# Kernel optimization log

Measured on AMD Instinct MI355X. Metric: run time of the kernel, lower is better.

The kernel has to match this reference:

```python
import jax, jax.numpy as jnp
import numpy as np
from jax import lax

K = 3  # deform kernel size (forced by shape consistency of the offset branch)


def conv2d(x, w, b, pad):
    y = lax.conv_general_dilated(x, w, (1, 1), [(pad, pad), (pad, pad)],
                                 dimension_numbers=('NCHW', 'OIHW', 'NCHW'))
    return y + b[None, :, None, None]


def deform_conv(x, offset, w):
    # Deformable conv v1, stride 1, pad 0, per-group offsets, zero outside borders.
    B, Cin, H, W = x.shape
    Cout = w.shape[0]
    Ho, Wo = H - K + 1, W - K + 1
    G = offset.shape[1] // (2 * K * K)  # num deformable groups (= cin // c_p_g)
    cpg = Cin // G
    # offset layout: [B, G, K*K, 2(y,x), Ho, Wo]
    off = offset.reshape(B, G, K * K, 2, Ho, Wo)
    ky = (jnp.arange(K * K) // K).astype(x.dtype)
    kx = (jnp.arange(K * K) % K).astype(x.dtype)
    py = off[:, :, :, 0] + jnp.arange(Ho, dtype=x.dtype)[None, None, None, :, None] + ky[None, None, :, None, None]
    px = off[:, :, :, 1] + jnp.arange(Wo, dtype=x.dtype)[None, None, None, None, :] + kx[None, None, :, None, None]
    y0 = jnp.floor(py)
    x0 = jnp.floor(px)
    fy = (py - y0)[..., None]  # [B,G,KK,Ho,Wo,1]
    fx = (px - x0)[..., None]
    y0i = y0.astype(jnp.int32)
    x0i = x0.astype(jnp.int32)
    xr = x.reshape(B, G, cpg, H, W)
    bi = jnp.arange(B)[:, None, None, None, None]
    gi = jnp.arange(G)[None, :, None, None, None]

    def gather(iy, ix):
        valid = (iy >= 0) & (iy < H) & (ix >= 0) & (ix < W)
        v = xr[bi, gi, :, jnp.clip(iy, 0, H - 1), jnp.clip(ix, 0, W - 1)]  # [B,G,KK,Ho,Wo,cpg]
        return v * valid[..., None].astype(x.dtype)

    v = ((1 - fy) * (1 - fx) * gather(y0i, x0i)
         + (1 - fy) * fx * gather(y0i, x0i + 1)
         + fy * (1 - fx) * gather(y0i + 1, x0i)
         + fy * fx * gather(y0i + 1, x0i + 1))
    # [B,G,KK,Ho,Wo,cpg] -> [B, Cin*K*K, Ho, Wo] matching weight layout [Cout, Cin, K, K]
    cols = v.transpose(0, 1, 5, 2, 3, 4).reshape(B, Cin * K * K, Ho, Wo)
    return jnp.einsum('ok,bkhw->bohw', w.reshape(Cout, -1), cols)


def setup_inputs() -> dict:
    key = jax.random.key(0)
    ks = jax.random.split(key, 8)
    B, cin, cout, H, W = 4, 64, 64, 130, 130
    s = 0.05
    x = jax.random.normal(ks[0], (B, cin, H, W), jnp.float32)
    w0 = jax.random.normal(ks[1], (cin, cin, 3, 3), jnp.float32) * s
    b0 = jnp.zeros((cin,), jnp.float32)
    w1 = jax.random.normal(ks[2], (cin // 2, cin, 1, 1), jnp.float32) * s
    b1 = jnp.zeros((cin // 2,), jnp.float32)
    w2 = jax.random.normal(ks[3], (cin // 2, cin // 2, 3, 3), jnp.float32) * s
    b2 = jnp.zeros((cin // 2,), jnp.float32)
    off_ch = cin * 2 * K * K  # c_p_g = 1 -> G = cin
    w3 = jax.random.normal(ks[4], (off_ch, cin // 2, 1, 1), jnp.float32) * s
    b3 = jnp.zeros((off_ch,), jnp.float32)
    wd = jax.random.normal(ks[5], (cout, cin, K, K), jnp.float32) * s
    return {"x": x, "w0": w0, "b0": b0, "w1": w1, "b1": b1, "w2": w2, "b2": b2,
            "w3": w3, "b3": b3, "wd": wd}


def reference(x, w0, b0, w1, b1, w2, b2, w3, b3, wd):
    t = conv2d(x, w0, b0, 0)                                   # [B,cin,H-2,W-2]
    t = lax.reduce_window(t, -jnp.inf, lax.max, (1, 1, 2, 2), (1, 1, 2, 2), 'VALID')
    t = conv2d(t, w1, b1, 0)
    t = conv2d(t, w2, b2, 1)
    t = conv2d(t, w3, b3, 0)                                   # offset logits
    t = jnp.repeat(jnp.repeat(t, 2, axis=2), 2, axis=3)        # nearest x2 upsample
    return deform_conv(x, t, wd)
```

## Files before the change

kernel.cpp:

```cpp
#include <hip/hip_runtime.h>
#include <hip/hip_bf16.h>
#include <hip/hip_fp16.h>


#define HX 130
#define WX 130

typedef short bf16x8 __attribute__((ext_vector_type(8)));
typedef _Float16 f16x8 __attribute__((ext_vector_type(8)));
typedef float f32x4 __attribute__((ext_vector_type(4)));

static __device__ __forceinline__ unsigned short f2bf(float f) {
    unsigned u = __float_as_uint(f);
    unsigned r = u + 0x7fff + ((u >> 16) & 1);
    return (unsigned short)(r >> 16);
}

static __device__ __forceinline__ int aoff320(int row, int col) {
    return row * 320 + ((((col >> 3) ^ (row & 7))) << 3) + (col & 7);
}

static __device__ __forceinline__ int aoff192(int row, int col) {
    return row * 192 + ((((col >> 3) ^ (row & 7))) << 3) + (col & 7);
}

__global__ __launch_bounds__(256) void k_wdt(const float* __restrict__ wd,
                                             const float* __restrict__ w3,
                                             const float* __restrict__ w0,
                                             const float* __restrict__ w2,
                                             unsigned short* __restrict__ wdtb,
                                             __half* __restrict__ w3h,
                                             unsigned short* __restrict__ w0b,
                                             unsigned short* __restrict__ w2b) {
    int idx = blockIdx.x * 256 + threadIdx.x;
    if (idx < 36864) {
        int o = idx / 576;
        int rem = idx - o * 576;
        int c = rem / 9;
        int kk = rem - c * 9;
        int h = c >> 5;
        int c5 = c & 31;
        int col = (c5 >> 4) * 144 + ((c5 >> 3) & 1) * 72 + (c5 & 7) * 9 + kk;
        wdtb[(size_t)(h * 64 + o) * 288 + col] = f2bf(wd[idx]);
        if (idx < 16) wdtb[36864 + idx] = 0;
    } else if (idx < 73728) {
        int i2 = idx - 36864;
        w3h[i2] = __float2half_rn(w3[i2]);
    } else if (idx < 114688) {
        int i3 = idx - 73728;
        int row = i3 / 160;
        int col = i3 - row * 160;
        int cig = row >> 6, oc = row & 63;
        unsigned short v = 0;
        if (col < 144) {
            int ci = (col * 57) >> 9;
            int kk = col - ci * 9;
            v = f2bf(w0[(size_t)(oc * 64 + cig * 16 + ci) * 9 + kk]);
        }
        w0b[i3] = v;
    } else {
        int i4 = idx - 114688;
        int row = i4 / 160;
        int col = i4 - row * 160;
        int cig = row >> 5, oc = row & 31;
        unsigned short v = 0;
        if (col < 144) {
            int ci = (col * 57) >> 9;
            int kk = col - ci * 9;
            v = f2bf(w2[(size_t)(oc * 32 + cig * 16 + ci) * 9 + kk]);
        }
        w2b[i4] = v;
    }
}

__global__ __launch_bounds__(256, 4) void k_conv0_mfma(const float* __restrict__ x,
                                                       const unsigned short* __restrict__ w0b,
                                                       const float* __restrict__ b0,
                                                       float* __restrict__ p1) {
    int blk = blockIdx.x;
    int tx = blk & 15;
    int ty = (blk >> 4) & 15;
    int b = blk >> 8;
    int tid = threadIdx.x;
    int w = tid >> 6;
    int lane = tid & 63;
    int lm = lane & 15;
    int lq = lane >> 4;
    int oy0 = ty * 8, ox0 = tx * 8;

    __shared__ __align__(16) unsigned short alds[64 * 192];
    __shared__ __align__(16) float xlds[1600];

    f32x4 acc[4];
    #pragma unroll
    for (int n = 0; n < 4; ++n) acc[n] = (f32x4){0.f, 0.f, 0.f, 0.f};

    if (tid < 128) {
        *(bf16x8*)&alds[aoff192(tid >> 1, 144 + (tid & 1) * 8)] =
            (bf16x8){0, 0, 0, 0, 0, 0, 0, 0};
    }

    const float* xb = x + (size_t)(b * 64) * (HX * WX) + oy0 * WX + ox0;
    int apx = tid >> 2;
    int acq = tid & 3;
    int py = apx >> 3, pxx = apx & 7;

    for (int cig = 0; cig < 4; ++cig) {
        #pragma unroll
        for (int j = 0; j < 7; ++j) {
            int i = tid + j * 256;
            if (i < 1600) {
                int ci = i / 100;
                int rem = i - ci * 100;
                int rr = rem / 10, cc = rem - rr * 10;
                xlds[i] = xb[(size_t)(cig * 16 + ci) * (HX * WX) + rr * WX + cc];
            }
        }
        __syncthreads();
        #pragma unroll
        for (int jj = 0; jj < 36; ++jj) {
            int col = acq * 36 + jj;
            int ci = (col * 57) >> 9;
            int kk = col - ci * 9;
            int ky = kk / 3, kx = kk - ky * 3;
            alds[aoff192(apx, col)] =
                f2bf(xlds[ci * 100 + (py + ky) * 10 + (pxx + kx)]);
        }
        __syncthreads();
        int arow = w * 16 + lm;
        const unsigned short* bbase = w0b + (size_t)cig * 64 * 160;
        #pragma unroll
        for (int ks = 0; ks < 5; ++ks) {
            bf16x8 a = *(const bf16x8*)&alds[aoff192(arow, ks * 32 + lq * 8)];
            #pragma unroll
            for (int n = 0; n < 4; ++n) {
                bf16x8 bb = *(const bf16x8*)(bbase + (size_t)(n * 16 + lm) * 160
                                             + ks * 32 + lq * 8);
                acc[n] = __builtin_amdgcn_mfma_f32_16x16x32_bf16(a, bb, acc[n], 0, 0, 0);
            }
        }
    }

    __syncthreads();
    float* dlds = (float*)alds;
    #pragma unroll
    for (int n = 0; n < 4; ++n) {
        int oc = n * 16 + lm;
        #pragma unroll
        for (int r = 0; r < 4; ++r) {
            int px = w * 16 + lq * 4 + r;
            dlds[oc * 65 + px] = acc[n][r];
        }
    }
    __syncthreads();
    {
        int oc = tid >> 2;
        int ppy = tid & 3;
        float bo = b0[oc];
        float4 o4;
        #pragma unroll
        for (int ppx = 0; ppx < 4; ++ppx) {
            const float* dp = &dlds[oc * 65 + (2 * ppy) * 8 + 2 * ppx];
            float m = fmaxf(fmaxf(dp[0], dp[1]), fmaxf(dp[8], dp[9])) + bo;
            ((float*)&o4)[ppx] = m;
        }
        *(float4*)(p1 + (((size_t)b * 64 + oc) * 64 + ty * 4 + ppy) * 64 + tx * 4) = o4;
    }
}

__global__ __launch_bounds__(256) void k_conv1x1_a(const float* __restrict__ p1,
                                                   const float* __restrict__ w1,
                                                   const float* __restrict__ b1,
                                                   float* __restrict__ t2) {
    int blk = blockIdx.x;
    int qt = blk & 3;
    int cog = (blk >> 2) & 15;
    int b = blk >> 6;
    int q = qt * 256 + threadIdx.x;
    float4 acc[2];
    #pragma unroll
    for (int i = 0; i < 2; ++i) {
        float bv = b1[cog * 2 + i];
        acc[i] = make_float4(bv, bv, bv, bv);
    }
    const float* ip = p1 + (size_t)b * 64 * 4096 + q * 4;
    for (int ci = 0; ci < 64; ++ci) {
        float4 v = *(const float4*)(ip + (size_t)ci * 4096);
        #pragma unroll
        for (int i = 0; i < 2; ++i) {
            float wv = w1[(cog * 2 + i) * 64 + ci];
            acc[i].x += wv * v.x; acc[i].y += wv * v.y;
            acc[i].z += wv * v.z; acc[i].w += wv * v.w;
        }
    }
    float* op = t2 + (size_t)b * 32 * 4096 + q * 4;
    #pragma unroll
    for (int i = 0; i < 2; ++i)
        *(float4*)(op + (size_t)(cog * 2 + i) * 4096) = acc[i];
}

__global__ __launch_bounds__(256, 4) void k_conv3_mfma(const float* __restrict__ t2,
                                                       const unsigned short* __restrict__ w2b,
                                                       const float* __restrict__ b2,
                                                       float* __restrict__ t3) {
    int blk = blockIdx.x;
    int tx = blk & 7;
    int ty = (blk >> 3) & 7;
    int b = blk >> 6;
    int tid = threadIdx.x;
    int w = tid >> 6;
    int lane = tid & 63;
    int lm = lane & 15;
    int lq = lane >> 4;
    int oy0 = ty * 8, ox0 = tx * 8;

    __shared__ __align__(16) unsigned short alds[64 * 192];
    __shared__ __align__(16) float xlds[1600];

    f32x4 acc[2];
    #pragma unroll
    for (int n = 0; n < 2; ++n) acc[n] = (f32x4){0.f, 0.f, 0.f, 0.f};

    if (tid < 128) {
        *(bf16x8*)&alds[aoff192(tid >> 1, 144 + (tid & 1) * 8)] =
            (bf16x8){0, 0, 0, 0, 0, 0, 0, 0};
    }

    const float* tb = t2 + (size_t)(b * 32) * 4096;
    int apx = tid >> 2;
    int acq = tid & 3;
    int py = apx >> 3, pxx = apx & 7;

    for (int cig = 0; cig < 2; ++cig) {
        #pragma unroll
        for (int j = 0; j < 7; ++j) {
            int i = tid + j * 256;
            if (i < 1600) {
                int ci = i / 100;
                int rem = i - ci * 100;
                int rr = rem / 10, cc = rem - rr * 10;
                int gy = oy0 + rr - 1, gx = ox0 + cc - 1;
                bool ok = (gy >= 0) & (gy < 64) & (gx >= 0) & (gx < 64);
                xlds[i] = ok ? tb[(size_t)(cig * 16 + ci) * 4096 + gy * 64 + gx]
                             : 0.f;
            }
        }
        __syncthreads();
        #pragma unroll
        for (int jj = 0; jj < 36; ++jj) {
            int col = acq * 36 + jj;
            int ci = (col * 57) >> 9;
            int kk = col - ci * 9;
            int ky = kk / 3, kx = kk - ky * 3;
            alds[aoff192(apx, col)] =
                f2bf(xlds[ci * 100 + (py + ky) * 10 + (pxx + kx)]);
        }
        __syncthreads();
        int arow = w * 16 + lm;
        const unsigned short* bbase = w2b + (size_t)cig * 32 * 160;
        #pragma unroll
        for (int ks = 0; ks < 5; ++ks) {
            bf16x8 a = *(const bf16x8*)&alds[aoff192(arow, ks * 32 + lq * 8)];
            #pragma unroll
            for (int n = 0; n < 2; ++n) {
                bf16x8 bb = *(const bf16x8*)(bbase + (size_t)(n * 16 + lm) * 160
                                             + ks * 32 + lq * 8);
                acc[n] = __builtin_amdgcn_mfma_f32_16x16x32_bf16(a, bb, acc[n], 0, 0, 0);
            }
        }
    }

    __syncthreads();
    float* dlds = (float*)alds;
    #pragma unroll
    for (int n = 0; n < 2; ++n) {
        int oc = n * 16 + lm;
        #pragma unroll
        for (int r = 0; r < 4; ++r) {
            int px = w * 16 + lq * 4 + r;
            dlds[oc * 65 + px] = acc[n][r];
        }
    }
    __syncthreads();
    {
        int oc = tid >> 3;
        int r = tid & 7;
        float bo = b2[oc];
        const float* dp = &dlds[oc * 65 + r * 8];
        float* op = t3 + ((size_t)(b * 32 + oc) * 64 + oy0 + r) * 64 + ox0;
        float4 a4 = make_float4(dp[0] + bo, dp[1] + bo, dp[2] + bo, dp[3] + bo);
        float4 b4 = make_float4(dp[4] + bo, dp[5] + bo, dp[6] + bo, dp[7] + bo);
        *(float4*)(op) = a4;
        *(float4*)(op + 4) = b4;
    }
}

__global__ __launch_bounds__(256, 3) void k_deform(const float* __restrict__ x,
                                                   const float* __restrict__ t3,
                                                   const __half* __restrict__ w3h,
                                                   const float* __restrict__ b3,
                                                   const unsigned short* __restrict__ wdtb,
                                                   float* __restrict__ out) {
    int blk = blockIdx.x;
    int b = blk & 3;
    int strip = blk >> 2;
    int tid = threadIdx.x;
    int po0 = strip * 16;
    int qy = po0 >> 6;
    int qx0 = po0 & 63;
    int w = tid >> 6;
    int lane = tid & 63;
    int lm = lane & 15;
    int lq = lane >> 4;
    int tq = tid & 15;
    int kb = tid >> 4;

    __shared__ __align__(16) unsigned short alds[64 * 320];
    __shared__ __align__(16) __half2 soff[2304];
    __shared__ __align__(16) _Float16 st3t[16 * 40];

    f32x4 acc[4];
    #pragma unroll
    for (int n = 0; n < 4; ++n) acc[n] = (f32x4){0.f, 0.f, 0.f, 0.f};

    const float* xb = x + (size_t)b * 64 * HX * WX;
    float fybase = (float)(2 * qy);
    float fxbase = (float)(2 * (qx0 + tq));

    {
        int px = tid & 15, ci0 = tid >> 4;
        const float* t3p = t3 + (size_t)b * 32 * 4096 + (qy * 64 + qx0 + px);
        st3t[px * 40 + ci0]      = (_Float16)t3p[(size_t)ci0 * 4096];
        st3t[px * 40 + ci0 + 16] = (_Float16)t3p[(size_t)(ci0 + 16) * 4096];
    }
    __syncthreads();
    const f16x8 bfrag = *(const f16x8*)&st3t[lm * 40 + lq * 8];

    for (int h = 0; h < 2; ++h) {
        #pragma unroll 1
        for (int sl = 0; sl < 2; ++sl) {
            int s = h * 2 + sl;
            __syncthreads();

            #pragma unroll
            for (int rep = 0; rep < 5; ++rep) {
                int t = rep * 4 + w;
                if (rep == 4) { if (w >= 2) break; t = 16 + w; }
                const f16x8 afrag = *(const f16x8*)((const _Float16*)w3h
                        + (size_t)(s * 288 + t * 16 + lm) * 32 + lq * 8);
                f32x4 d = __builtin_amdgcn_mfma_f32_16x16x32_f16(
                        afrag, bfrag, (f32x4){0.f, 0.f, 0.f, 0.f}, 0, 0, 0);
                float4 bq = *(const float4*)(b3 + s * 288 + t * 16 + lq * 4);
                int p0 = (t * 8 + lq * 2) * 16 + lm;
                soff[p0]      = __floats2half2_rn(d[0] + bq.x, d[1] + bq.y);
                soff[p0 + 16] = __floats2half2_rn(d[2] + bq.z, d[3] + bq.w);
            }
            __syncthreads();

            __half2 o2h[9];
            #pragma unroll
            for (int it = 0; it < 9; ++it)
                o2h[it] = soff[it * 256 + tid];
            #pragma unroll
            for (int it = 0; it < 9; ++it) {
                int kcol = it * 16 + kb;
                int lc = kcol >= 72;
                int ckk = kcol - 72 * lc;
                int ch = (ckk * 57) >> 9;
                int kk = ckk - ch * 9;
                int c = s * 16 + lc * 8 + ch;
                int clocal = sl * 144 + kcol;
                float2 off = __half22float2(o2h[it]);
                float py = off.x + fybase + (float)(kk / 3);
                float px = off.y + fxbase + (float)(kk % 3);
                float y0f = floorf(py), x0f = floorf(px);
                float fy = py - y0f, fx = px - x0f;
                int y0 = (int)y0f, x0 = (int)x0f;
                const float* xp = xb + (size_t)c * (HX * WX);
                float tv[3][3];
                bool fastok = (y0 >= 0) & (y0 <= HX - 3) & (x0 >= 0) & (x0 <= WX - 3);
                if (__all(fastok)) {
                    int xe = x0 & ~1;
                    int odd = x0 & 1;
                    const float* rp = xp + y0 * WX + xe;
                    #pragma unroll
                    for (int r = 0; r < 3; ++r) {
                        float2 A = *(const float2*)(rp);
                        float2 B = *(const float2*)(rp + 2);
                        tv[r][0] = odd ? A.y : A.x;
                        tv[r][1] = odd ? B.x : A.y;
                        tv[r][2] = odd ? B.y : B.x;
                        rp += WX;
                    }
                } else {
                    #pragma unroll
                    for (int r = 0; r < 3; ++r) {
                        int yy = y0 + r;
                        bool vy = (yy >= 0) & (yy < HX);
                        int yc = min(max(yy, 0), HX - 1);
                        #pragma unroll
                        for (int sx = 0; sx < 3; ++sx) {
                            int xx = x0 + sx;
                            bool vx = (xx >= 0) & (xx < WX);
                            int xc = min(max(xx, 0), WX - 1);
                            float val = xp[yc * WX + xc];
                            tv[r][sx] = (vy & vx) ? val : 0.f;
                        }
                    }
                }
                float h0[3], h1[3];
                #pragma unroll
                for (int r = 0; r < 3; ++r) {
                    h0[r] = tv[r][0] + fx * (tv[r][1] - tv[r][0]);
                    h1[r] = tv[r][1] + fx * (tv[r][2] - tv[r][1]);
                }
                alds[aoff320(0 * 16 + tq, clocal)] = f2bf(h0[0] + fy * (h0[1] - h0[0]));
                alds[aoff320(1 * 16 + tq, clocal)] = f2bf(h1[0] + fy * (h1[1] - h1[0]));
                alds[aoff320(2 * 16 + tq, clocal)] = f2bf(h0[1] + fy * (h0[2] - h0[1]));
                alds[aoff320(3 * 16 + tq, clocal)] = f2bf(h1[1] + fy * (h1[2] - h1[1]));
            }
        }
        __syncthreads();

        int arow = w * 16 + lm;
        const unsigned short* bbase = wdtb + (size_t)(h * 64) * 288;
        #pragma unroll
        for (int ks = 0; ks < 9; ++ks) {
            bf16x8 a = *(const bf16x8*)&alds[aoff320(arow, ks * 32 + lq * 8)];
            #pragma unroll
            for (int n = 0; n < 4; ++n) {
                bf16x8 bb = *(const bf16x8*)(bbase + (size_t)(n * 16 + lm) * 288
                                             + ks * 32 + lq * 8);
                acc[n] = __builtin_amdgcn_mfma_f32_16x16x32_bf16(a, bb, acc[n], 0, 0, 0);
            }
        }
    }

    __syncthreads();
    float* dlds = (float*)alds;
    #pragma unroll
    for (int n = 0; n < 4; ++n) {
        int oc = n * 16 + lm;
        #pragma unroll
        for (int r = 0; r < 4; ++r) {
            int px = w * 16 + lq * 4 + r;
            dlds[oc * 65 + px] = acc[n][r];
        }
    }
    __syncthreads();
    {
        int oc = tid >> 2;
        int sy = (tid >> 1) & 1;
        int qh = (tid & 1) * 8;
        float* orow = out + (((size_t)b * 64 + oc) * 128 + 2 * qy + sy) * 128 + 2 * qx0;
        const float* d0 = &dlds[oc * 65 + (sy * 2 + 0) * 16];
        const float* d1 = &dlds[oc * 65 + (sy * 2 + 1) * 16];
        #pragma unroll
        for (int i = 0; i < 8; ++i) {
            int q = qh + i;
            *(float2*)(orow + 2 * q) = make_float2(d0[q], d1[q]);
        }
    }
}

extern "C" void kernel_launch(void* const* d_in, const int* in_sizes, int n_in,
                              void* d_out, int out_size, void* d_ws, size_t ws_size,
                              hipStream_t stream) {
    const float* x  = (const float*)d_in[0];
    const float* w0 = (const float*)d_in[1];
    const float* b0 = (const float*)d_in[2];
    const float* w1 = (const float*)d_in[3];
    const float* b1 = (const float*)d_in[4];
    const float* w2 = (const float*)d_in[5];
    const float* b2 = (const float*)d_in[6];
    const float* w3 = (const float*)d_in[7];
    const float* b3 = (const float*)d_in[8];
    const float* wd = (const float*)d_in[9];
    float* out = (float*)d_out;

    float* ws = (float*)d_ws;
    float* p1    = ws;
    float* t2    = p1 + 1048576;
    float* t3    = t2 + 524288;
    unsigned short* wdtb = (unsigned short*)(t3 + 524288);
    __half* w3h = (__half*)(wdtb + 36880);
    unsigned short* w0b = (unsigned short*)(w3h + 36864);
    unsigned short* w2b = w0b + 40960;

    k_wdt<<<488, 256, 0, stream>>>(wd, w3, w0, w2, wdtb, w3h, w0b, w2b);
    k_conv0_mfma<<<1024, 256, 0, stream>>>(x, w0b, b0, p1);
    k_conv1x1_a<<<256, 256, 0, stream>>>(p1, w1, b1, t2);
    k_conv3_mfma<<<256, 256, 0, stream>>>(t2, w2b, b2, t3);
    k_deform<<<1024, 256, 0, stream>>>(x, t3, w3h, b3, wdtb, out);
}
```

Baseline: 223.5 us.

## Fuse 1x1 conv into 3x3 conv with MFMA and halve deform LDS staging

Result: no change. 226.9 us (+1.5%).

```diff
diff --git a/kernel.cpp b/kernel.cpp
--- a/kernel.cpp
+++ b/kernel.cpp
@@ -16,22 +16,24 @@
     return (unsigned short)(r >> 16);
 }
 
-static __device__ __forceinline__ int aoff320(int row, int col) {
-    return row * 320 + ((((col >> 3) ^ (row & 7))) << 3) + (col & 7);
-}
-
 static __device__ __forceinline__ int aoff192(int row, int col) {
     return row * 192 + ((((col >> 3) ^ (row & 7))) << 3) + (col & 7);
+}
+
+static __device__ __forceinline__ int aoff80(int row, int col) {
+    return row * 80 + ((((col >> 3) ^ (row & 7))) << 3) + (col & 7);
 }
 
 __global__ __launch_bounds__(256) void k_wdt(const float* __restrict__ wd,
                                              const float* __restrict__ w3,
                                              const float* __restrict__ w0,
                                              const float* __restrict__ w2,
+                                             const float* __restrict__ w1,
                                              unsigned short* __restrict__ wdtb,
                                              __half* __restrict__ w3h,
                                              unsigned short* __restrict__ w0b,
-                                             unsigned short* __restrict__ w2b) {
+                                             unsigned short* __restrict__ w2b,
+                                             unsigned short* __restrict__ w1b) {
     int idx = blockIdx.x * 256 + threadIdx.x;
     if (idx < 36864) {
         int o = idx / 576;
@@ -58,7 +60,7 @@
             v = f2bf(w0[(size_t)(oc * 64 + cig * 16 + ci) * 9 + kk]);
         }
         w0b[i3] = v;
-    } else {
+    } else if (idx < 124928) {
         int i4 = idx - 114688;
         int row = i4 / 160;
         int col = i4 - row * 160;
@@ -70,6 +72,9 @@
             v = f2bf(w2[(size_t)(oc * 32 + cig * 16 + ci) * 9 + kk]);
         }
         w2b[i4] = v;
+    } else {
+        int i5 = idx - 124928;
+        w1b[i5] = f2bf(w1[i5]);
     }
 }
 
@@ -168,41 +173,12 @@
     }
 }
 
-__global__ __launch_bounds__(256) void k_conv1x1_a(const float* __restrict__ p1,
-                                                   const float* __restrict__ w1,
-                                                   const float* __restrict__ b1,
-                                                   float* __restrict__ t2) {
-    int blk = blockIdx.x;
-    int qt = blk & 3;
-    int cog = (blk >> 2) & 15;
-    int b = blk >> 6;
-    int q = qt * 256 + threadIdx.x;
-    float4 acc[2];
-    #pragma unroll
-    for (int i = 0; i < 2; ++i) {
-        float bv = b1[cog * 2 + i];
-        acc[i] = make_float4(bv, bv, bv, bv);
-    }
-    const float* ip = p1 + (size_t)b * 64 * 4096 + q * 4;
-    for (int ci = 0; ci < 64; ++ci) {
-        float4 v = *(const float4*)(ip + (size_t)ci * 4096);
-        #pragma unroll
-        for (int i = 0; i < 2; ++i) {
-            float wv = w1[(cog * 2 + i) * 64 + ci];
-            acc[i].x += wv * v.x; acc[i].y += wv * v.y;
-            acc[i].z += wv * v.z; acc[i].w += wv * v.w;
-        }
-    }
-    float* op = t2 + (size_t)b * 32 * 4096 + q * 4;
-    #pragma unroll
-    for (int i = 0; i < 2; ++i)
-        *(float4*)(op + (size_t)(cog * 2 + i) * 4096) = acc[i];
-}
-
-__global__ __launch_bounds__(256, 4) void k_conv3_mfma(const float* __restrict__ t2,
-                                                       const unsigned short* __restrict__ w2b,
-                                                       const float* __restrict__ b2,
-                                                       float* __restrict__ t3) {
+__global__ __launch_bounds__(256) void k_conv13(const float* __restrict__ p1,
+                                                const unsigned short* __restrict__ w1b,
+                                                const float* __restrict__ b1,
+                                                const unsigned short* __restrict__ w2b,
+                                                const float* __restrict__ b2,
+                                                float* __restrict__ t3) {
     int blk = blockIdx.x;
     int tx = blk & 7;
     int ty = (blk >> 3) & 7;
@@ -214,37 +190,65 @@
     int lq = lane >> 4;
     int oy0 = ty * 8, ox0 = tx * 8;
 
-    __shared__ __align__(16) unsigned short alds[64 * 192];
-    __shared__ __align__(16) float xlds[1600];
-
-    f32x4 acc[2];
-    #pragma unroll
-    for (int n = 0; n < 2; ++n) acc[n] = (f32x4){0.f, 0.f, 0.f, 0.f};
-
+    __shared__ __align__(16) float t2b[32 * 100];
+    __shared__ __align__(16) unsigned short areg[64 * 192];
+
+    const float* pb = p1 + (size_t)(b * 64) * 4096;
+    #pragma unroll
+    for (int j = 0; j < 25; ++j) {
+        int i = tid + j * 256;
+        int ci = i / 100;
+        int pp = i - ci * 100;
+        int rr = pp / 10, cc = pp - rr * 10;
+        int gy = oy0 + rr - 1, gx = ox0 + cc - 1;
+        bool ok = (gy >= 0) & (gy < 64) & (gx >= 0) & (gx < 64);
+        float v = ok ? pb[(size_t)ci * 4096 + gy * 64 + gx] : 0.f;
+        areg[aoff80(pp, ci)] = f2bf(v);
+    }
+    __syncthreads();
+
+    #pragma unroll
+    for (int s7 = 0; s7 < 2; ++s7) {
+        int rt = w + s7 * 4;
+        if (rt < 7) {
+            f32x4 a1[2];
+            a1[0] = (f32x4){0.f, 0.f, 0.f, 0.f};
+            a1[1] = (f32x4){0.f, 0.f, 0.f, 0.f};
+            #pragma unroll
+            for (int ks = 0; ks < 2; ++ks) {
+                bf16x8 a = *(const bf16x8*)&areg[aoff80(rt * 16 + lm, ks * 32 + lq * 8)];
+                #pragma unroll
+                for (int n = 0; n < 2; ++n) {
+                    bf16x8 bb = *(const bf16x8*)(w1b + (size_t)(n * 16 + lm) * 64
+                                                 + ks * 32 + lq * 8);
+                    a1[n] = __builtin_amdgcn_mfma_f32_16x16x32_bf16(a, bb, a1[n], 0, 0, 0);
+                }
+            }
+            #pragma unroll
+            for (int n = 0; n < 2; ++n) {
+                int oc = n * 16 + lm;
+                float bv = b1[oc];
+                #pragma unroll
+                for (int r = 0; r < 4; ++r) {
+                    int px = rt * 16 + lq * 4 + r;
+                    if (px < 100) t2b[oc * 100 + px] = a1[n][r] + bv;
+                }
+            }
+        }
+    }
+    __syncthreads();
+
+    int apx = tid >> 2, acq = tid & 3;
+    int py = apx >> 3, pxx = apx & 7;
+    f32x4 acc3[2];
+    acc3[0] = (f32x4){0.f, 0.f, 0.f, 0.f};
+    acc3[1] = (f32x4){0.f, 0.f, 0.f, 0.f};
     if (tid < 128) {
-        *(bf16x8*)&alds[aoff192(tid >> 1, 144 + (tid & 1) * 8)] =
+        *(bf16x8*)&areg[aoff192(tid >> 1, 144 + (tid & 1) * 8)] =
             (bf16x8){0, 0, 0, 0, 0, 0, 0, 0};
     }
-
-    const float* tb = t2 + (size_t)(b * 32) * 4096;
-    int apx = tid >> 2;
-    int acq = tid & 3;
-    int py = apx >> 3, pxx = apx & 7;
-
+    #pragma unroll 1
     for (int cig = 0; cig < 2; ++cig) {
-        #pragma unroll
-        for (int j = 0; j < 7; ++j) {
-            int i = tid + j * 256;
-            if (i < 1600) {
-                int ci = i / 100;
-                int rem = i - ci * 100;
-                int rr = rem / 10, cc = rem - rr * 10;
-                int gy = oy0 + rr - 1, gx = ox0 + cc - 1;
-                bool ok = (gy >= 0) & (gy < 64) & (gx >= 0) & (gx < 64);
-                xlds[i] = ok ? tb[(size_t)(cig * 16 + ci) * 4096 + gy * 64 + gx]
-                             : 0.f;
-            }
-        }
         __syncthreads();
         #pragma unroll
         for (int jj = 0; jj < 36; ++jj) {
@@ -252,33 +256,33 @@
             int ci = (col * 57) >> 9;
             int kk = col - ci * 9;
             int ky = kk / 3, kx = kk - ky * 3;
-            alds[aoff192(apx, col)] =
-                f2bf(xlds[ci * 100 + (py + ky) * 10 + (pxx + kx)]);
+            areg[aoff192(apx, col)] =
+                f2bf(t2b[(cig * 16 + ci) * 100 + (py + ky) * 10 + (pxx + kx)]);
         }
         __syncthreads();
         int arow = w * 16 + lm;
         const unsigned short* bbase = w2b + (size_t)cig * 32 * 160;
         #pragma unroll
         for (int ks = 0; ks < 5; ++ks) {
-            bf16x8 a = *(const bf16x8*)&alds[aoff192(arow, ks * 32 + lq * 8)];
+            bf16x8 a = *(const bf16x8*)&areg[aoff192(arow, ks * 32 + lq * 8)];
             #pragma unroll
             for (int n = 0; n < 2; ++n) {
                 bf16x8 bb = *(const bf16x8*)(bbase + (size_t)(n * 16 + lm) * 160
                                              + ks * 32 + lq * 8);
-                acc[n] = __builtin_amdgcn_mfma_f32_16x16x32_bf16(a, bb, acc[n], 0, 0, 0);
-            }
-        }
-    }
-
-    __syncthreads();
-    float* dlds = (float*)alds;
+                acc3[n] = __builtin_amdgcn_mfma_f32_16x16x32_bf16(a, bb, acc3[n], 0, 0, 0);
+            }
+        }
+    }
+
+    __syncthreads();
+    float* dlds = (float*)areg;
     #pragma unroll
     for (int n = 0; n < 2; ++n) {
         int oc = n * 16 + lm;
         #pragma unroll
         for (int r = 0; r < 4; ++r) {
             int px = w * 16 + lq * 4 + r;
-            dlds[oc * 65 + px] = acc[n][r];
+            dlds[oc * 65 + px] = acc3[n][r];
         }
     }
     __syncthreads();
@@ -315,7 +319,7 @@
     int tq = tid & 15;
     int kb = tid >> 4;
 
-    __shared__ __align__(16) unsigned short alds[64 * 320];
+    __shared__ __align__(16) unsigned short alds[64 * 192];
     __shared__ __align__(16) __half2 soff[2304];
     __shared__ __align__(16) _Float16 st3t[16 * 40];
 
@@ -333,6 +337,10 @@
         st3t[px * 40 + ci0]      = (_Float16)t3p[(size_t)ci0 * 4096];
         st3t[px * 40 + ci0 + 16] = (_Float16)t3p[(size_t)(ci0 + 16) * 4096];
     }
+    if (tid < 128) {
+        *(bf16x8*)&alds[aoff192(tid >> 1, 144 + (tid & 1) * 8)] =
+            (bf16x8){0, 0, 0, 0, 0, 0, 0, 0};
+    }
     __syncthreads();
     const f16x8 bfrag = *(const f16x8*)&st3t[lm * 40 + lq * 8];
 
@@ -340,7 +348,6 @@
         #pragma unroll 1
         for (int sl = 0; sl < 2; ++sl) {
             int s = h * 2 + sl;
-            __syncthreads();
 
             #pragma unroll
             for (int rep = 0; rep < 5; ++rep) {
@@ -369,7 +376,7 @@
                 int ch = (ckk * 57) >> 9;
                 int kk = ckk - ch * 9;
                 int c = s * 16 + lc * 8 + ch;
-                int clocal = sl * 144 + kcol;
+                int clocal = kcol;
                 float2 off = __half22float2(o2h[it]);
                 float py = off.x + fybase + (float)(kk / 3);
                 float px = off.y + fxbase + (float)(kk % 3);
@@ -414,24 +421,24 @@
                     h0[r] = tv[r][0] + fx * (tv[r][1] - tv[r][0]);
                     h1[r] = tv[r][1] + fx * (tv[r][2] - tv[r][1]);
                 }
-                alds[aoff320(0 * 16 + tq, clocal)] = f2bf(h0[0] + fy * (h0[1] - h0[0]));
-                alds[aoff320(1 * 16 + tq, clocal)] = f2bf(h1[0] + fy * (h1[1] - h1[0]));
-                alds[aoff320(2 * 16 + tq, clocal)] = f2bf(h0[1] + fy * (h0[2] - h0[1]));
-                alds[aoff320(3 * 16 + tq, clocal)] = f2bf(h1[1] + fy * (h1[2] - h1[1]));
-            }
-        }
-        __syncthreads();
-
-        int arow = w * 16 + lm;
-        const unsigned short* bbase = wdtb + (size_t)(h * 64) * 288;
-        #pragma unroll
-        for (int ks = 0; ks < 9; ++ks) {
-            bf16x8 a = *(const bf16x8*)&alds[aoff320(arow, ks * 32 + lq * 8)];
-            #pragma unroll
-            for (int n = 0; n < 4; ++n) {
-                bf16x8 bb = *(const bf16x8*)(bbase + (size_t)(n * 16 + lm) * 288
-                                             + ks * 32 + lq * 8);
-                acc[n] = __builtin_amdgcn_mfma_f32_16x16x32_bf16(a, bb, acc[n], 0, 0, 0);
+                alds[aoff192(0 * 16 + tq, clocal)] = f2bf(h0[0] + fy * (h0[1] - h0[0]));
+                alds[aoff192(1 * 16 + tq, clocal)] = f2bf(h1[0] + fy * (h1[1] - h1[0]));
+                alds[aoff192(2 * 16 + tq, clocal)] = f2bf(h0[1] + fy * (h0[2] - h0[1]));
+                alds[aoff192(3 * 16 + tq, clocal)] = f2bf(h1[1] + fy * (h1[2] - h1[1]));
+            }
+            __syncthreads();
+
+            int arow = w * 16 + lm;
+            const unsigned short* bbase = wdtb + (size_t)(h * 64) * 288 + sl * 144;
+            #pragma unroll
+            for (int ks = 0; ks < 5; ++ks) {
+                bf16x8 a = *(const bf16x8*)&alds[aoff192(arow, ks * 32 + lq * 8)];
+                #pragma unroll
+                for (int n = 0; n < 4; ++n) {
+                    bf16x8 bb = *(const bf16x8*)(bbase + (size_t)(n * 16 + lm) * 288
+                                                 + ks * 32 + lq * 8);
+                    acc[n] = __builtin_amdgcn_mfma_f32_16x16x32_bf16(a, bb, acc[n], 0, 0, 0);
+                }
             }
         }
     }
@@ -480,16 +487,15 @@
 
     float* ws = (float*)d_ws;
     float* p1    = ws;
-    float* t2    = p1 + 1048576;
-    float* t3    = t2 + 524288;
+    float* t3    = p1 + 1048576;
     unsigned short* wdtb = (unsigned short*)(t3 + 524288);
     __half* w3h = (__half*)(wdtb + 36880);
     unsigned short* w0b = (unsigned short*)(w3h + 36864);
     unsigned short* w2b = w0b + 40960;
-
-    k_wdt<<<488, 256, 0, stream>>>(wd, w3, w0, w2, wdtb, w3h, w0b, w2b);
+    unsigned short* w1b = w2b + 10240;
+
+    k_wdt<<<496, 256, 0, stream>>>(wd, w3, w0, w2, w1, wdtb, w3h, w0b, w2b, w1b);
     k_conv0_mfma<<<1024, 256, 0, stream>>>(x, w0b, b0, p1);
-    k_conv1x1_a<<<256, 256, 0, stream>>>(p1, w1, b1, t2);
-    k_conv3_mfma<<<256, 256, 0, stream>>>(t2, w2b, b2, t3);
+    k_conv13<<<256, 256, 0, stream>>>(p1, w1b, b1, w2b, b2, t3);
     k_deform<<<1024, 256, 0, stream>>>(x, t3, w3h, b3, wdtb, out);
 }
```
